# Kernel optimization log

Measured on AMD Instinct MI355X. Metric: run time of the kernel, lower is better.

Reference implementation:

```python
import jax, jax.numpy as jnp
import numpy as np
from jax import lax

N_QUANTIZE = 256
N_AUX = 28
N_RESCH = 512
N_SKIPCH = 256
KS = 2
DILATIONS = [2 ** i for i in range(10)] * 3  # 30 layers
L = len(DILATIONS)


def _causal_conv(x, w, b, d):
    # x: (B, Cin, T), w: (Cout, Cin, KS) torch Conv1d layout, left-pad => causal
    pad = (w.shape[-1] - 1) * d
    y = lax.conv_general_dilated(x, w, window_strides=(1,), padding=[(pad, 0)],
                                 rhs_dilation=(d,),
                                 dimension_numbers=('NCH', 'OIH', 'NCH'))
    return y + b[None, :, None]


def _conv1x1(x, w, b):
    # x: (B, Cin, T), w: (Cout, Cin)
    return jnp.einsum('oi,bit->bot', w, x) + b[None, :, None]


def setup_inputs() -> dict:
    key = jax.random.key(0)
    ks = jax.random.split(key, 20)
    B, T = 2, 8000
    s = 0.05
    rn = lambda k, shape: (jax.random.normal(k, shape, jnp.float32) * s)
    inp = {
        'x': jax.random.randint(ks[0], (B, T), 0, N_QUANTIZE),
        'h': jax.random.normal(ks[1], (B, N_AUX, T), jnp.float32),
        'causal_w': rn(ks[2], (N_RESCH, N_QUANTIZE, KS)),
        'causal_b': rn(ks[3], (N_RESCH,)),
        'dil_sig_w': rn(ks[4], (L, N_RESCH, N_RESCH, KS)),
        'dil_sig_b': rn(ks[5], (L, N_RESCH)),
        'dil_tanh_w': rn(ks[6], (L, N_RESCH, N_RESCH, KS)),
        'dil_tanh_b': rn(ks[7], (L, N_RESCH)),
        'aux_sig_w': rn(ks[8], (L, N_RESCH, N_AUX)),
        'aux_sig_b': rn(ks[9], (L, N_RESCH)),
        'aux_tanh_w': rn(ks[10], (L, N_RESCH, N_AUX)),
        'aux_tanh_b': rn(ks[11], (L, N_RESCH)),
        'skip_w': rn(ks[12], (L, N_SKIPCH, N_RESCH)),
        'skip_b': rn(ks[13], (L, N_SKIPCH)),
        'res_w': rn(ks[14], (L, N_RESCH, N_RESCH)),
        'res_b': rn(ks[15], (L, N_RESCH)),
        'post1_w': rn(ks[16], (N_SKIPCH, N_SKIPCH)),
        'post1_b': rn(ks[17], (N_SKIPCH,)),
        'post2_w': rn(ks[18], (N_QUANTIZE, N_SKIPCH)),
        'post2_b': rn(ks[19], (N_QUANTIZE,)),
    }
    return inp


def reference(x, h, causal_w, causal_b, dil_sig_w, dil_sig_b, dil_tanh_w, dil_tanh_b,
              aux_sig_w, aux_sig_b, aux_tanh_w, aux_tanh_b, skip_w, skip_b,
              res_w, res_b, post1_w, post1_b, post2_w, post2_b):
    B, T = x.shape
    # _preprocess: onehot (B,T,Q) -> (B,Q,T), then causal conv
    oh = jax.nn.one_hot(x % N_QUANTIZE, N_QUANTIZE, dtype=jnp.float32).transpose(0, 2, 1)
    out = _causal_conv(oh, causal_w, causal_b, 1)  # (B, n_resch, T)
    skip_sum = jnp.zeros((B, N_SKIPCH, T), jnp.float32)
    for l, d in enumerate(DILATIONS):
        sig = _causal_conv(out, dil_sig_w[l], dil_sig_b[l], d) + _conv1x1(h, aux_sig_w[l], aux_sig_b[l])
        tan = _causal_conv(out, dil_tanh_w[l], dil_tanh_b[l], d) + _conv1x1(h, aux_tanh_w[l], aux_tanh_b[l])
        z = jax.nn.sigmoid(sig) * jnp.tanh(tan)
        skip_sum = skip_sum + _conv1x1(z, skip_w[l], skip_b[l])
        out = _conv1x1(z, res_w[l], res_b[l]) + out
    # _postprocess: relu -> 1x1 -> relu -> 1x1 -> (B, T, n_quantize)
    y = jax.nn.relu(skip_sum)
    y = jax.nn.relu(_conv1x1(y, post1_w, post1_b))
    y = _conv1x1(y, post2_w, post2_b)
    return y.transpose(0, 2, 1)
```

## Files before the change

### kernel.cpp

```cpp
#include <hip/hip_runtime.h>
#include <math.h>

#define T_LEN 8000
#define BATCH 2
#define CCH 512
#define SKP 256
#define AUXP 32
#define NQ 256
#define NLAYER 30
#define PADF 512
#define TPAD 8192
#define ROWS (PADF + TPAD)
#define HROWS TPAD

typedef unsigned short hfu;
typedef unsigned int u32;
typedef __attribute__((ext_vector_type(8))) _Float16 half8;
typedef __attribute__((ext_vector_type(4))) float f32x4;

#define GLOAD16(g, l)                                                          \
  __builtin_amdgcn_global_load_lds(                                            \
      (const __attribute__((address_space(1))) void*)(g),                      \
      (__attribute__((address_space(3))) void*)(l), 16, 0, 0)

__device__ inline hfu hfbits(float f) {
  union { _Float16 h; hfu u; } x;
  x.h = (_Float16)f;
  return x.u;
}
__device__ inline u32 pk2(float a, float b) {
  return (u32)hfbits(a) | ((u32)hfbits(b) << 16);
}
__device__ inline uint4 pk8(const float f[8]) {
  return make_uint4(pk2(f[0], f[1]), pk2(f[2], f[3]), pk2(f[4], f[5]), pk2(f[6], f[7]));
}
__device__ inline int ldsL(int row, int ck) {
  return ((row >> 1) << 3) + ((((ck) ^ ((row >> 1) & 3)) << 1) | (row & 1));
}

__global__ __launch_bounds__(256) void zero16(uint4* p, int n) {
  for (int i = blockIdx.x * 256 + threadIdx.x; i < n; i += gridDim.x * 256)
    p[i] = make_uint4(0u, 0u, 0u, 0u);
}

__global__ __launch_bounds__(256) void cvt_dil(const float* __restrict__ in, hfu* __restrict__ out) {
  const long NG = (long)NLAYER * CCH * (CCH / 4);
  for (long g = (long)blockIdx.x * 256 + threadIdx.x; g < NG; g += (long)gridDim.x * 256) {
    const int i4 = (int)(g & 127) * 4;
    const int o = (int)((g >> 7) & 511);
    const int l = (int)(g >> 16);
    const float* pp = in + (((size_t)l * CCH + o) * CCH + i4) * 2;
    float4 f0 = *(const float4*)pp;
    float4 f1 = *(const float4*)(pp + 4);
    uint2 t0 = make_uint2(pk2(f0.x, f0.z), pk2(f1.x, f1.z));
    uint2 t1 = make_uint2(pk2(f0.y, f0.w), pk2(f1.y, f1.w));
    hfu* ob = out + ((size_t)l * 2 * CCH + o) * CCH + i4;
    *(uint2*)ob = t0;
    *(uint2*)(ob + (size_t)CCH * CCH) = t1;
  }
}

__global__ __launch_bounds__(256) void cvt_skipres(const float* __restrict__ skw,
                                                   const float* __restrict__ rsw,
                                                   hfu* __restrict__ out) {
  const long NG = (long)NLAYER * 768 * (CCH / 4);
  for (long g = (long)blockIdx.x * 256 + threadIdx.x; g < NG; g += (long)gridDim.x * 256) {
    const int i4 = (int)(g & 127) * 4;
    const int r = (int)((g >> 7) % 768);
    const int l = (int)(g / (128 * 768));
    const float* src = (r < SKP) ? (skw + ((size_t)l * SKP + r) * CCH + i4)
                                 : (rsw + ((size_t)l * CCH + (r - SKP)) * CCH + i4);
    float4 f = *(const float4*)src;
    *(uint2*)(out + ((size_t)l * 768 + r) * CCH + i4) = make_uint2(pk2(f.x, f.y), pk2(f.z, f.w));
  }
}

__global__ __launch_bounds__(256) void cvt_aux(const float* __restrict__ in, hfu* __restrict__ out) {
  const int N = NLAYER * CCH * AUXP;
  for (int i = blockIdx.x * 256 + threadIdx.x; i < N; i += gridDim.x * 256) {
    const int j = i & 31;
    const int o = (i >> 5) & 511;
    const int l = i >> 14;
    float v = (j < 28) ? in[((size_t)l * CCH + o) * 28 + j] : 0.f;
    out[i] = hfbits(v);
  }
}

__global__ __launch_bounds__(256) void cvt_copy(const float* __restrict__ in, hfu* __restrict__ out, int n) {
  for (int i = blockIdx.x * 256 + threadIdx.x; i < n; i += gridDim.x * 256)
    out[i] = hfbits(in[i]);
}

__global__ __launch_bounds__(256) void cvt_cwt(const float* __restrict__ cw, float* __restrict__ out) {
  const int N = 2 * NQ * CCH;
  for (int i = blockIdx.x * 256 + threadIdx.x; i < N; i += gridDim.x * 256) {
    const int tap = i >> 17;
    const int r = i & 131071;
    const int xq = r >> 9;
    const int o = r & 511;
    out[i] = cw[((size_t)o * NQ + xq) * 2 + tap];
  }
}

__global__ __launch_bounds__(256) void htrans_kernel(const float* __restrict__ h, hfu* __restrict__ hbf) {
  const int b = blockIdx.y;
  const int t = blockIdx.x * 64 + (threadIdx.x & 63);
  const int j0 = threadIdx.x >> 6;
#pragma unroll
  for (int j = j0; j < AUXP; j += 4) {
    float v = (j < 28 && t < T_LEN) ? h[((size_t)b * 28 + j) * T_LEN + t] : 0.f;
    hbf[((size_t)b * HROWS + t) * AUXP + j] = hfbits(v);
  }
}

template <int PRE>
__global__ __launch_bounds__(256) void embed_kernel(const int* __restrict__ x,
                                                    const float* __restrict__ cwt,
                                                    const float* __restrict__ cb,
                                                    float* __restrict__ outf,
                                                    hfu* __restrict__ outb) {
  const int b = blockIdx.y;
  const int t = blockIdx.x * 4 + (threadIdx.x >> 6);
  const int o = (threadIdx.x & 63) * 8;
  const int xc = x[(size_t)b * T_LEN + t] & 255;
  const int xp = (t > 0) ? (x[(size_t)b * T_LEN + t - 1] & 255) : 0;
  const float won = (t > 0) ? 1.f : 0.f;
  const float* c1 = cwt + 131072 + (size_t)xc * CCH + o;
  const float* c0 = cwt + (size_t)xp * CCH + o;
  float v[8];
#pragma unroll
  for (int j = 0; j < 8; ++j) v[j] = cb[o + j] + c1[j] + won * c0[j];
  if (PRE) {
    *(uint4*)&outb[((size_t)b * ROWS + PADF + t) * CCH + o] = pk8(v);
  } else {
    float* po = outf + ((size_t)b * ROWS + PADF + t) * CCH + o;
    *(float4*)po = make_float4(v[0], v[1], v[2], v[3]);
    *(float4*)(po + 4) = make_float4(v[4], v[5], v[6], v[7]);
  }
}

template <int PRE>
__global__ __launch_bounds__(512, 2) void gate_kernel(
    const hfu* __restrict__ actb, const float* __restrict__ actf,
    const hfu* __restrict__ hbf,
    const void* __restrict__ wsp, const void* __restrict__ wtp,
    const hfu* __restrict__ auxs, const hfu* __restrict__ auxt,
    const float* __restrict__ bs1, const float* __restrict__ bs2,
    const float* __restrict__ bt1, const float* __restrict__ bt2,
    hfu* __restrict__ z, int d) {
  __shared__ uint4 sm[4096];
  const int tid = threadIdx.x;
  const int lane = tid & 63, wid = tid >> 6;
  const int wm = wid >> 2, wn = wid & 3;
  const int lr = lane & 15, lq = lane >> 4;

  const int n = blockIdx.x;
  const int f = (n & 7) * 32 + (n >> 3);
  const int tt = f >> 3, inner = f & 7;
  const int o0 = (inner >> 1) * 128;
  const int b = inner & 1;
  const int t0 = tt * 256;

  f32x4 accS[4][4] = {};
  f32x4 accT[4][4] = {};

  auto stage = [&](int ih, int p) {
    const int base = p * 2048;
    const int pr = tid >> 3, w = tid & 7;
    const int row = (pr << 1) | (w & 1);
    const int ck = (w >> 1) ^ (pr & 3);
    if (ih < 32) {
      const int tau = (ih < 16) ? 1 : 0;
      const int koff = (ih & 15) * 32;
      if (PRE) {
        const size_t wo = ((size_t)tau * CCH + o0 + row) * CCH + koff + ck * 8;
        GLOAD16((const hfu*)wsp + wo, &sm[base + tid]);
        GLOAD16((const hfu*)wtp + wo, &sm[base + 512 + tid]);
#pragma unroll
        for (int c = 0; c < 2; ++c) {
          const int s = c * 512 + tid;
          const int pr2 = s >> 3, w2 = s & 7;
          const int row2 = (pr2 << 1) | (w2 & 1);
          const int ck2 = (w2 >> 1) ^ (pr2 & 3);
          const hfu* ar = actb + ((size_t)b * ROWS + PADF + t0 + row2 - (tau ? 0 : d)) * CCH + koff + ck2 * 8;
          GLOAD16(ar, &sm[base + 1024 + s]);
        }
      } else {
        const float* wsf = (const float*)wsp;
        const float* wtf = (const float*)wtp;
        const size_t fb = ((size_t)(o0 + row) * CCH + koff + ck * 8) * 2;
        float vs[8], vt[8];
#pragma unroll
        for (int j = 0; j < 4; ++j) {
          float4 fs = *(const float4*)&wsf[fb + j * 4];
          float4 ft = *(const float4*)&wtf[fb + j * 4];
          vs[2 * j] = tau ? fs.y : fs.x;
          vs[2 * j + 1] = tau ? fs.w : fs.z;
          vt[2 * j] = tau ? ft.y : ft.x;
          vt[2 * j + 1] = tau ? ft.w : ft.z;
        }
        sm[base + tid] = pk8(vs);
        sm[base + 512 + tid] = pk8(vt);
#pragma unroll
        for (int c = 0; c < 2; ++c) {
          const int s = c * 512 + tid;
          const int pr2 = s >> 3, w2 = s & 7;
          const int row2 = (pr2 << 1) | (w2 & 1);
          const int ck2 = (w2 >> 1) ^ (pr2 & 3);
          const float* ar = actf + ((size_t)b * ROWS + PADF + t0 + row2 - (tau ? 0 : d)) * CCH + koff + ck2 * 8;
          float4 f0 = *(const float4*)&ar[0];
          float4 f1 = *(const float4*)&ar[4];
          float vb[8] = {f0.x, f0.y, f0.z, f0.w, f1.x, f1.y, f1.z, f1.w};
          sm[base + 1024 + s] = pk8(vb);
        }
      }
    } else {
      if (PRE) {
        GLOAD16(auxs + (size_t)(o0 + row) * AUXP + ck * 8, &sm[base + tid]);
        GLOAD16(auxt + (size_t)(o0 + row) * AUXP + ck * 8, &sm[base + 512 + tid]);
      } else {
        sm[base + tid] = *(const uint4*)&auxs[(size_t)(o0 + row) * AUXP + ck * 8];
        sm[base + 512 + tid] = *(const uint4*)&auxt[(size_t)(o0 + row) * AUXP + ck * 8];
      }
#pragma unroll
      for (int c = 0; c < 2; ++c) {
        const int s = c * 512 + tid;
        const int pr2 = s >> 3, w2 = s & 7;
        const int row2 = (pr2 << 1) | (w2 & 1);
        const int ck2 = (w2 >> 1) ^ (pr2 & 3);
        if (PRE)
          GLOAD16(hbf + ((size_t)b * HROWS + t0 + row2) * AUXP + ck2 * 8, &sm[base + 1024 + s]);
        else
          sm[base + 1024 + s] = *(const uint4*)&hbf[((size_t)b * HROWS + t0 + row2) * AUXP + ck2 * 8];
      }
    }
  };

  auto compute = [&](int p) {
    const int base = p * 2048;
    half8 af[4], ag[4], bv[4];
#pragma unroll
    for (int mr = 0; mr < 4; ++mr) {
      const int row = wm * 64 + mr * 16 + lr;
      const int idx = ldsL(row, lq);
      af[mr] = *(const half8*)&sm[base + idx];
      ag[mr] = *(const half8*)&sm[base + 512 + idx];
    }
#pragma unroll
    for (int nr = 0; nr < 4; ++nr) {
      const int row = wn * 64 + nr * 16 + lr;
      bv[nr] = *(const half8*)&sm[base + 1024 + ldsL(row, lq)];
    }
#pragma unroll
    for (int mr = 0; mr < 4; ++mr)
#pragma unroll
      for (int nr = 0; nr < 4; ++nr) {
        accS[mr][nr] = __builtin_amdgcn_mfma_f32_16x16x32_f16(af[mr], bv[nr], accS[mr][nr], 0, 0, 0);
        accT[mr][nr] = __builtin_amdgcn_mfma_f32_16x16x32_f16(ag[mr], bv[nr], accT[mr][nr], 0, 0, 0);
      }
  };

  if (PRE) {
    stage(0, 0);
    for (int ih = 0; ih < 33; ++ih) {
      if (ih < 32) {
        stage(ih + 1, (ih + 1) & 1);
        asm volatile("s_waitcnt vmcnt(4)" ::: "memory");
      } else {
        asm volatile("s_waitcnt vmcnt(0)" ::: "memory");
      }
      __builtin_amdgcn_s_barrier();
      __builtin_amdgcn_sched_barrier(0);
      __builtin_amdgcn_s_setprio(1);
      compute(ih & 1);
      __builtin_amdgcn_s_setprio(0);
      __builtin_amdgcn_sched_barrier(0);
      __builtin_amdgcn_s_barrier();
    }
  } else {
    for (int ih = 0; ih < 33; ++ih) {
      stage(ih, ih & 1);
      __syncthreads();
      compute(ih & 1);
      __syncthreads();
    }
  }

#pragma unroll
  for (int mr = 0; mr < 4; ++mr) {
    const int ob = o0 + wm * 64 + mr * 16 + lq * 4;
    float4 x1 = *(const float4*)&bs1[ob];
    float4 x2 = *(const float4*)&bs2[ob];
    float4 y1 = *(const float4*)&bt1[ob];
    float4 y2 = *(const float4*)&bt2[ob];
    const float sb[4] = {x1.x + x2.x, x1.y + x2.y, x1.z + x2.z, x1.w + x2.w};
    const float tb[4] = {y1.x + y2.x, y1.y + y2.y, y1.z + y2.z, y1.w + y2.w};
#pragma unroll
    for (int nr = 0; nr < 4; ++nr) {
      const int t = t0 + wn * 64 + nr * 16 + lr;
      float zv[4];
#pragma unroll
      for (int j = 0; j < 4; ++j) {
        float sv = accS[mr][nr][j] + sb[j];
        float tv = accT[mr][nr][j] + tb[j];
        float sg = __builtin_amdgcn_rcpf(1.f + __expf(-sv));
        float e2 = __expf(2.f * tv);
        float th = 1.f - 2.f * __builtin_amdgcn_rcpf(e2 + 1.f);
        zv[j] = sg * th;
      }
      *(uint2*)&z[((size_t)b * HROWS + t) * CCH + ob] = make_uint2(pk2(zv[0], zv[1]), pk2(zv[2], zv[3]));
    }
  }
}

template <int PRE>
__global__ __launch_bounds__(512, 4) void update_kernel(
    const hfu* __restrict__ z, const void* __restrict__ wp,
    const float* __restrict__ skwf, const float* __restrict__ rswf,
    const float* __restrict__ skb, const float* __restrict__ rsb,
    float* __restrict__ skip, float* __restrict__ outf, hfu* __restrict__ outb) {
  __shared__ uint4 sm[2048];
  const int tid = threadIdx.x;
  const int lane = tid & 63, wid = tid >> 6;
  const int wm = wid >> 1, wn = wid & 1;
  const int lr = lane & 15, lq = lane >> 4;

  const int n = blockIdx.x;
  const int xcd = n & 7, j = n >> 3;
  const int ttl = j / 12, inner = j % 12;
  const int tt = xcd * 8 + ttl;
  if (tt > 62) return;
  const int rg = inner >> 1, b = inner & 1;
  const int r0 = rg * 128;
  const int t0 = tt * 128;

  f32x4 acc[2][4] = {};

  auto stage_u = [&](int ih, int p) {
    const int base = p * 1024;
    const int pr = tid >> 3, w = tid & 7;
    const int row = (pr << 1) | (w & 1);
    const int ck = (w >> 1) ^ (pr & 3);
    const int k0 = ih * 32;
    if (PRE) {
      GLOAD16((const hfu*)wp + (size_t)(r0 + row) * CCH + k0 + ck * 8, &sm[base + tid]);
      GLOAD16(z + ((size_t)b * HROWS + t0 + row) * CCH + k0 + ck * 8, &sm[base + 512 + tid]);
    } else {
      const int R = r0 + row;
      const float* src = (R < SKP) ? (skwf + (size_t)R * CCH + k0 + ck * 8)
                                   : (rswf + (size_t)(R - SKP) * CCH + k0 + ck * 8);
      float4 f0 = *(const float4*)&src[0];
      float4 f1 = *(const float4*)&src[4];
      float v[8] = {f0.x, f0.y, f0.z, f0.w, f1.x, f1.y, f1.z, f1.w};
      sm[base + tid] = pk8(v);
      sm[base + 512 + tid] = *(const uint4*)&z[((size_t)b * HROWS + t0 + row) * CCH + k0 + ck * 8];
    }
  };

  auto compute_u = [&](int p) {
    const int base = p * 1024;
    half8 av[2], bv[4];
#pragma unroll
    for (int mr = 0; mr < 2; ++mr) {
      const int row = wm * 32 + mr * 16 + lr;
      av[mr] = *(const half8*)&sm[base + ldsL(row, lq)];
    }
#pragma unroll
    for (int nr = 0; nr < 4; ++nr) {
      const int row = wn * 64 + nr * 16 + lr;
      bv[nr] = *(const half8*)&sm[base + 512 + ldsL(row, lq)];
    }
#pragma unroll
    for (int mr = 0; mr < 2; ++mr)
#pragma unroll
      for (int nr = 0; nr < 4; ++nr)
        acc[mr][nr] = __builtin_amdgcn_mfma_f32_16x16x32_f16(av[mr], bv[nr], acc[mr][nr], 0, 0, 0);
  };

  if (PRE) {
    stage_u(0, 0);
    for (int ih = 0; ih < 16; ++ih) {
      if (ih < 15) {
        stage_u(ih + 1, (ih + 1) & 1);
        asm volatile("s_waitcnt vmcnt(2)" ::: "memory");
      } else {
        asm volatile("s_waitcnt vmcnt(0)" ::: "memory");
      }
      __builtin_amdgcn_s_barrier();
      __builtin_amdgcn_sched_barrier(0);
      __builtin_amdgcn_s_setprio(1);
      compute_u(ih & 1);
      __builtin_amdgcn_s_setprio(0);
      __builtin_amdgcn_sched_barrier(0);
      __builtin_amdgcn_s_barrier();
    }
  } else {
    for (int ih = 0; ih < 16; ++ih) {
      stage_u(ih, ih & 1);
      __syncthreads();
      compute_u(ih & 1);
      __syncthreads();
    }
  }

  const bool iskip = (r0 < SKP);
#pragma unroll
  for (int mr = 0; mr < 2; ++mr) {
    const int R = r0 + wm * 32 + mr * 16 + lq * 4;
#pragma unroll
    for (int nr = 0; nr < 4; ++nr) {
      const int t = t0 + wn * 64 + nr * 16 + lr;
      if (t < T_LEN) {
        if (iskip) {
          float4 bb = *(const float4*)&skb[R];
          float4* p = (float4*)&skip[((size_t)b * T_LEN + t) * SKP + R];
          float4 v = *p;
          v.x += acc[mr][nr][0] + bb.x;
          v.y += acc[mr][nr][1] + bb.y;
          v.z += acc[mr][nr][2] + bb.z;
          v.w += acc[mr][nr][3] + bb.w;
          *p = v;
        } else {
          const int rr = R - SKP;
          float4 bb = *(const float4*)&rsb[rr];
          if (PRE) {
            hfu* pb = &outb[((size_t)b * ROWS + PADF + t) * CCH + rr];
            uint2 old = *(uint2*)pb;
            const _Float16* hp = (const _Float16*)&old;
            float v0 = (float)hp[0] + acc[mr][nr][0] + bb.x;
            float v1 = (float)hp[1] + acc[mr][nr][1] + bb.y;
            float v2 = (float)hp[2] + acc[mr][nr][2] + bb.z;
            float v3 = (float)hp[3] + acc[mr][nr][3] + bb.w;
            *(uint2*)pb = make_uint2(pk2(v0, v1), pk2(v2, v3));
          } else {
            float4* p = (float4*)&outf[((size_t)b * ROWS + PADF + t) * CCH + rr];
            float4 v = *p;
            v.x += acc[mr][nr][0] + bb.x;
            v.y += acc[mr][nr][1] + bb.y;
            v.z += acc[mr][nr][2] + bb.z;
            v.w += acc[mr][nr][3] + bb.w;
            *p = v;
          }
        }
      }
    }
  }
}

__global__ __launch_bounds__(256, 2) void post1_kernel(const float* __restrict__ skip,
                                                       const hfu* __restrict__ w,
                                                       const float* __restrict__ bias,
                                                       hfu* __restrict__ y1) {
  __shared__ uint4 sm[2048];
  uint4* sA = sm;
  uint4* sB = sm + 1024;
  const int tid = threadIdx.x;
  const int lane = tid & 63, wid = tid >> 6;
  const int wm = wid >> 1, wn = wid & 1;
  const int lr = lane & 15, lq = lane >> 4;
  const int t0 = blockIdx.x * 128;
  const int r0 = blockIdx.y * 128;
  const int b = blockIdx.z;
  f32x4 acc[4][4] = {};
  for (int kt = 0; kt < 4; ++kt) {
#pragma unroll
    for (int c = 0; c < 4; ++c) {
      const int cb = c * 256 + wid * 64;
      const int ch = cb + lane;
      const int ksub = ch >> 7, mn = ch & 127;
      const int k0 = kt * 64 + ksub * 8;
      GLOAD16(w + (size_t)(r0 + mn) * SKP + k0, &sA[cb]);
      int row = t0 + mn;
      if (row > T_LEN - 1) row = T_LEN - 1;
      const float* src = skip + ((size_t)b * T_LEN + row) * SKP + k0;
      float4 f0 = *(const float4*)&src[0];
      float4 f1 = *(const float4*)&src[4];
      float v[8] = {fmaxf(f0.x, 0.f), fmaxf(f0.y, 0.f), fmaxf(f0.z, 0.f), fmaxf(f0.w, 0.f),
                    fmaxf(f1.x, 0.f), fmaxf(f1.y, 0.f), fmaxf(f1.z, 0.f), fmaxf(f1.w, 0.f)};
      sB[ch] = pk8(v);
    }
    __syncthreads();
#pragma unroll
    for (int ks = 0; ks < 2; ++ks) {
      const int kb = (ks * 4 + lq) * 128;
      half8 av[4], bv[4];
#pragma unroll
      for (int r = 0; r < 4; ++r) {
        av[r] = *(const half8*)&sA[kb + wm * 64 + r * 16 + lr];
        bv[r] = *(const half8*)&sB[kb + wn * 64 + r * 16 + lr];
      }
#pragma unroll
      for (int mr = 0; mr < 4; ++mr)
#pragma unroll
        for (int nr = 0; nr < 4; ++nr)
          acc[mr][nr] = __builtin_amdgcn_mfma_f32_16x16x32_f16(av[mr], bv[nr], acc[mr][nr], 0, 0, 0);
    }
    __syncthreads();
  }
#pragma unroll
  for (int mr = 0; mr < 4; ++mr) {
    const int ob = r0 + wm * 64 + mr * 16 + lq * 4;
    float4 bb = *(const float4*)&bias[ob];
    const float bs[4] = {bb.x, bb.y, bb.z, bb.w};
#pragma unroll
    for (int nr = 0; nr < 4; ++nr) {
      const int t = t0 + wn * 64 + nr * 16 + lr;
      float v[4];
#pragma unroll
      for (int j = 0; j < 4; ++j) v[j] = fmaxf(acc[mr][nr][j] + bs[j], 0.f);
      *(uint2*)&y1[((size_t)b * HROWS + t) * SKP + ob] = make_uint2(pk2(v[0], v[1]), pk2(v[2], v[3]));
    }
  }
}

__global__ __launch_bounds__(256, 2) void post2_kernel(const hfu* __restrict__ y1,
                                                       const hfu* __restrict__ w,
                                                       const float* __restrict__ bias,
                                                       float* __restrict__ outp) {
  __shared__ uint4 sm[2048];
  uint4* sA = sm;
  uint4* sB = sm + 1024;
  const int tid = threadIdx.x;
  const int lane = tid & 63, wid = tid >> 6;
  const int wm = wid >> 1, wn = wid & 1;
  const int lr = lane & 15, lq = lane >> 4;
  const int t0 = blockIdx.x * 128;
  const int r0 = blockIdx.y * 128;
  const int b = blockIdx.z;
  f32x4 acc[4][4] = {};
  for (int kt = 0; kt < 4; ++kt) {
#pragma unroll
    for (int c = 0; c < 4; ++c) {
      const int cb = c * 256 + wid * 64;
      const int ch = cb + lane;
      const int ksub = ch >> 7, mn = ch & 127;
      const int k0 = kt * 64 + ksub * 8;
      GLOAD16(w + (size_t)(r0 + mn) * SKP + k0, &sA[cb]);
      GLOAD16(y1 + ((size_t)b * HROWS + t0 + mn) * SKP + k0, &sB[cb]);
    }
    __syncthreads();
#pragma unroll
    for (int ks = 0; ks < 2; ++ks) {
      const int kb = (ks * 4 + lq) * 128;
      half8 av[4], bv[4];
#pragma unroll
      for (int r = 0; r < 4; ++r) {
        av[r] = *(const half8*)&sA[kb + wm * 64 + r * 16 + lr];
        bv[r] = *(const half8*)&sB[kb + wn * 64 + r * 16 + lr];
      }
#pragma unroll
      for (int mr = 0; mr < 4; ++mr)
#pragma unroll
        for (int nr = 0; nr < 4; ++nr)
          acc[mr][nr] = __builtin_amdgcn_mfma_f32_16x16x32_f16(av[mr], bv[nr], acc[mr][nr], 0, 0, 0);
    }
    __syncthreads();
  }
#pragma unroll
  for (int mr = 0; mr < 4; ++mr) {
    const int ob = r0 + wm * 64 + mr * 16 + lq * 4;
    float4 bb = *(const float4*)&bias[ob];
#pragma unroll
    for (int nr = 0; nr < 4; ++nr) {
      const int t = t0 + wn * 64 + nr * 16 + lr;
      if (t < T_LEN) {
        float4 v;
        v.x = acc[mr][nr][0] + bb.x;
        v.y = acc[mr][nr][1] + bb.y;
        v.z = acc[mr][nr][2] + bb.z;
        v.w = acc[mr][nr][3] + bb.w;
        *(float4*)&outp[((size_t)b * T_LEN + t) * NQ + ob] = v;
      }
    }
  }
}

extern "C" void kernel_launch(void* const* d_in, const int* in_sizes, int n_in,
                              void* d_out, int out_size, void* d_ws, size_t ws_size,
                              hipStream_t stream) {
  const int* x = (const int*)d_in[0];
  const float* h = (const float*)d_in[1];
  const float* causal_w = (const float*)d_in[2];
  const float* causal_b = (const float*)d_in[3];
  const float* dil_sig_w = (const float*)d_in[4];
  const float* dil_sig_b = (const float*)d_in[5];
  const float* dil_tanh_w = (const float*)d_in[6];
  const float* dil_tanh_b = (const float*)d_in[7];
  const float* aux_sig_w = (const float*)d_in[8];
  const float* aux_sig_b = (const float*)d_in[9];
  const float* aux_tanh_w = (const float*)d_in[10];
  const float* aux_tanh_b = (const float*)d_in[11];
  const float* skip_w = (const float*)d_in[12];
  const float* skip_b = (const float*)d_in[13];
  const float* res_w = (const float*)d_in[14];
  const float* res_b = (const float*)d_in[15];
  const float* post1_w = (const float*)d_in[16];
  const float* post1_b = (const float*)d_in[17];
  const float* post2_w = (const float*)d_in[18];
  const float* post2_b = (const float*)d_in[19];
  float* outp = (float*)d_out;

  char* p = (char*)d_ws;
  auto alloc = [&](size_t bytes) {
    char* r = p;
    p += (bytes + 255) & ~(size_t)255;
    return r;
  };
  float* outf = (float*)alloc((size_t)BATCH * ROWS * CCH * 4);
  float* skip = (float*)alloc((size_t)BATCH * T_LEN * SKP * 4);
  hfu* zb = (hfu*)alloc((size_t)BATCH * HROWS * CCH * 2);
  hfu* hbf = (hfu*)alloc((size_t)BATCH * HROWS * AUXP * 2);
  hfu* auxsb = (hfu*)alloc((size_t)NLAYER * CCH * AUXP * 2);
  hfu* auxtb = (hfu*)alloc((size_t)NLAYER * CCH * AUXP * 2);
  hfu* p1b = (hfu*)alloc((size_t)NQ * SKP * 2);
  hfu* p2b = (hfu*)alloc((size_t)NQ * SKP * 2);
  float* cwt = (float*)alloc((size_t)2 * NQ * CCH * 4);
  hfu* y1 = zb;
  hfu* outb = (hfu*)alloc((size_t)BATCH * ROWS * CCH * 2);
  hfu* dilS = (hfu*)alloc((size_t)NLAYER * 2 * CCH * CCH * 2);
  hfu* dilT = (hfu*)alloc((size_t)NLAYER * 2 * CCH * CCH * 2);
  hfu* wsr = (hfu*)alloc((size_t)NLAYER * 768 * CCH * 2);
  const bool pre = ((size_t)(p - (char*)d_ws) <= ws_size);

  cvt_aux<<<256, 256, 0, stream>>>(aux_sig_w, auxsb);
  cvt_aux<<<256, 256, 0, stream>>>(aux_tanh_w, auxtb);
  cvt_copy<<<64, 256, 0, stream>>>(post1_w, p1b, NQ * SKP);
  cvt_copy<<<64, 256, 0, stream>>>(post2_w, p2b, NQ * SKP);
  cvt_cwt<<<1024, 256, 0, stream>>>(causal_w, cwt);
  if (pre) {
    cvt_dil<<<2048, 256, 0, stream>>>(dil_sig_w, dilS);
    cvt_dil<<<2048, 256, 0, stream>>>(dil_tanh_w, dilT);
    cvt_skipres<<<2048, 256, 0, stream>>>(skip_w, res_w, wsr);
  }

  zero16<<<512, 256, 0, stream>>>((uint4*)skip, (int)((size_t)BATCH * T_LEN * SKP * 4 / 16));
  for (int b = 0; b < BATCH; ++b) {
    if (pre) {
      zero16<<<32, 256, 0, stream>>>((uint4*)(outb + (size_t)b * ROWS * CCH), PADF * CCH * 2 / 16);
      zero16<<<48, 256, 0, stream>>>((uint4*)(outb + ((size_t)b * ROWS + PADF + T_LEN) * CCH),
                                     (TPAD - T_LEN) * CCH * 2 / 16);
    } else {
      zero16<<<64, 256, 0, stream>>>((uint4*)(outf + (size_t)b * ROWS * CCH), PADF * CCH * 4 / 16);
      zero16<<<96, 256, 0, stream>>>((uint4*)(outf + ((size_t)b * ROWS + PADF + T_LEN) * CCH),
                                     (TPAD - T_LEN) * CCH * 4 / 16);
    }
  }

  htrans_kernel<<<dim3(128, 2), 256, 0, stream>>>(h, hbf);
  if (pre)
    embed_kernel<1><<<dim3(2000, 2), 256, 0, stream>>>(x, cwt, causal_b, nullptr, outb);
  else
    embed_kernel<0><<<dim3(2000, 2), 256, 0, stream>>>(x, cwt, causal_b, outf, nullptr);

  for (int l = 0; l < NLAYER; ++l) {
    const int d = 1 << (l % 10);
    if (pre) {
      gate_kernel<1><<<256, 512, 0, stream>>>(
          outb, nullptr, hbf, dilS + (size_t)l * 2 * CCH * CCH, dilT + (size_t)l * 2 * CCH * CCH,
          auxsb + (size_t)l * CCH * AUXP, auxtb + (size_t)l * CCH * AUXP,
          dil_sig_b + (size_t)l * CCH, aux_sig_b + (size_t)l * CCH,
          dil_tanh_b + (size_t)l * CCH, aux_tanh_b + (size_t)l * CCH, zb, d);
      update_kernel<1><<<768, 512, 0, stream>>>(
          zb, wsr + (size_t)l * 768 * CCH, nullptr, nullptr,
          skip_b + (size_t)l * SKP, res_b + (size_t)l * CCH, skip, nullptr, outb);
    } else {
      gate_kernel<0><<<256, 512, 0, stream>>>(
          nullptr, outf, hbf, dil_sig_w + (size_t)l * CCH * CCH * 2,
          dil_tanh_w + (size_t)l * CCH * CCH * 2,
          auxsb + (size_t)l * CCH * AUXP, auxtb + (size_t)l * CCH * AUXP,
          dil_sig_b + (size_t)l * CCH, aux_sig_b + (size_t)l * CCH,
          dil_tanh_b + (size_t)l * CCH, aux_tanh_b + (size_t)l * CCH, zb, d);
      update_kernel<0><<<768, 512, 0, stream>>>(
          zb, nullptr, skip_w + (size_t)l * SKP * CCH, res_w + (size_t)l * CCH * CCH,
          skip_b + (size_t)l * SKP, res_b + (size_t)l * CCH, skip, outf, nullptr);
    }
  }

  post1_kernel<<<dim3(63, 2, BATCH), 256, 0, stream>>>(skip, p1b, post1_b, y1);
  post2_kernel<<<dim3(63, 2, BATCH), 256, 0, stream>>>(y1, p2b, post2_b, outp);
}
```

Measured before the change: 2.166 ms.

## Double gate K-tile to 64 with dynamic LDS, store skip sum in fp16, fuse dil conversion

The gate kernel now stages 64-wide K chunks (16 dilated iterations plus one aux step instead of 33) into 128 KB of dynamic shared memory with a new XOR swizzle. This halves the number of barriers and pipeline steps per tile. The skip accumulator becomes fp16 in the pre-converted path, halving its read-modify-write traffic in every layer's update kernel, at some cost in accumulation precision. The two dilated-weight conversion launches are merged into one. The larger LDS footprint may lower occupancy from the declared 2 blocks per CU.

```diff
diff --git a/kernel.cpp b/kernel.cpp
--- a/kernel.cpp
+++ b/kernel.cpp
@@ -43,9 +43,15 @@
     p[i] = make_uint4(0u, 0u, 0u, 0u);
 }
 
-__global__ __launch_bounds__(256) void cvt_dil(const float* __restrict__ in, hfu* __restrict__ out) {
+__global__ __launch_bounds__(256) void cvt_dil2(const float* __restrict__ inS,
+                                                const float* __restrict__ inT,
+                                                hfu* __restrict__ outS, hfu* __restrict__ outT) {
   const long NG = (long)NLAYER * CCH * (CCH / 4);
-  for (long g = (long)blockIdx.x * 256 + threadIdx.x; g < NG; g += (long)gridDim.x * 256) {
+  for (long g2 = (long)blockIdx.x * 256 + threadIdx.x; g2 < 2 * NG; g2 += (long)gridDim.x * 256) {
+    const int sel = (int)(g2 >= NG);
+    const long g = sel ? (g2 - NG) : g2;
+    const float* in = sel ? inT : inS;
+    hfu* out = sel ? outT : outS;
     const int i4 = (int)(g & 127) * 4;
     const int o = (int)((g >> 7) & 511);
     const int l = (int)(g >> 16);
@@ -148,7 +154,7 @@
     const float* __restrict__ bs1, const float* __restrict__ bs2,
     const float* __restrict__ bt1, const float* __restrict__ bt2,
     hfu* __restrict__ z, int d) {
-  __shared__ uint4 sm[4096];
+  extern __shared__ uint4 smd[];
   const int tid = threadIdx.x;
   const int lane = tid & 63, wid = tid >> 6;
   const int wm = wid >> 2, wn = wid & 3;
@@ -164,30 +170,33 @@
   f32x4 accS[4][4] = {};
   f32x4 accT[4][4] = {};
 
-  auto stage = [&](int ih, int p) {
-    const int base = p * 2048;
-    const int pr = tid >> 3, w = tid & 7;
-    const int row = (pr << 1) | (w & 1);
-    const int ck = (w >> 1) ^ (pr & 3);
-    if (ih < 32) {
-      const int tau = (ih < 16) ? 1 : 0;
-      const int koff = (ih & 15) * 32;
-      if (PRE) {
+  auto stage_dil = [&](int ih, int p) {
+    const int base = p * 4096;
+    const int tau = (ih < 8) ? 1 : 0;
+    const int koff = (ih & 7) * 64;
+    if (PRE) {
+#pragma unroll
+      for (int c = 0; c < 2; ++c) {
+        const int s = c * 512 + tid;
+        const int row = s >> 3, ck = (s & 7) ^ (row & 7);
         const size_t wo = ((size_t)tau * CCH + o0 + row) * CCH + koff + ck * 8;
-        GLOAD16((const hfu*)wsp + wo, &sm[base + tid]);
-        GLOAD16((const hfu*)wtp + wo, &sm[base + 512 + tid]);
-#pragma unroll
-        for (int c = 0; c < 2; ++c) {
-          const int s = c * 512 + tid;
-          const int pr2 = s >> 3, w2 = s & 7;
-          const int row2 = (pr2 << 1) | (w2 & 1);
-          const int ck2 = (w2 >> 1) ^ (pr2 & 3);
-          const hfu* ar = actb + ((size_t)b * ROWS + PADF + t0 + row2 - (tau ? 0 : d)) * CCH + koff + ck2 * 8;
-          GLOAD16(ar, &sm[base + 1024 + s]);
-        }
-      } else {
-        const float* wsf = (const float*)wsp;
-        const float* wtf = (const float*)wtp;
+        GLOAD16((const hfu*)wsp + wo, &smd[base + s]);
+        GLOAD16((const hfu*)wtp + wo, &smd[base + 1024 + s]);
+      }
+#pragma unroll
+      for (int c = 0; c < 4; ++c) {
+        const int s = c * 512 + tid;
+        const int row = s >> 3, ck = (s & 7) ^ (row & 7);
+        const hfu* ar = actb + ((size_t)b * ROWS + PADF + t0 + row - (tau ? 0 : d)) * CCH + koff + ck * 8;
+        GLOAD16(ar, &smd[base + 2048 + s]);
+      }
+    } else {
+      const float* wsf = (const float*)wsp;
+      const float* wtf = (const float*)wtp;
+#pragma unroll
+      for (int c = 0; c < 2; ++c) {
+        const int s = c * 512 + tid;
+        const int row = s >> 3, ck = (s & 7) ^ (row & 7);
         const size_t fb = ((size_t)(o0 + row) * CCH + koff + ck * 8) * 2;
         float vs[8], vt[8];
 #pragma unroll
@@ -199,57 +208,86 @@
           vt[2 * j] = tau ? ft.y : ft.x;
           vt[2 * j + 1] = tau ? ft.w : ft.z;
         }
-        sm[base + tid] = pk8(vs);
-        sm[base + 512 + tid] = pk8(vt);
-#pragma unroll
-        for (int c = 0; c < 2; ++c) {
-          const int s = c * 512 + tid;
-          const int pr2 = s >> 3, w2 = s & 7;
-          const int row2 = (pr2 << 1) | (w2 & 1);
-          const int ck2 = (w2 >> 1) ^ (pr2 & 3);
-          const float* ar = actf + ((size_t)b * ROWS + PADF + t0 + row2 - (tau ? 0 : d)) * CCH + koff + ck2 * 8;
-          float4 f0 = *(const float4*)&ar[0];
-          float4 f1 = *(const float4*)&ar[4];
-          float vb[8] = {f0.x, f0.y, f0.z, f0.w, f1.x, f1.y, f1.z, f1.w};
-          sm[base + 1024 + s] = pk8(vb);
+        smd[base + s] = pk8(vs);
+        smd[base + 1024 + s] = pk8(vt);
+      }
+#pragma unroll
+      for (int c = 0; c < 4; ++c) {
+        const int s = c * 512 + tid;
+        const int row = s >> 3, ck = (s & 7) ^ (row & 7);
+        const float* ar = actf + ((size_t)b * ROWS + PADF + t0 + row - (tau ? 0 : d)) * CCH + koff + ck * 8;
+        float4 f0 = *(const float4*)&ar[0];
+        float4 f1 = *(const float4*)&ar[4];
+        float vb[8] = {f0.x, f0.y, f0.z, f0.w, f1.x, f1.y, f1.z, f1.w};
+        smd[base + 2048 + s] = pk8(vb);
+      }
+    }
+  };
+
+  auto stage_aux = [&](int p) {
+    const int base = p * 4096;
+    {
+      const int row = tid >> 2, ck = (tid & 3) ^ (row & 3);
+      if (PRE) {
+        GLOAD16(auxs + (size_t)(o0 + row) * AUXP + ck * 8, &smd[base + tid]);
+        GLOAD16(auxt + (size_t)(o0 + row) * AUXP + ck * 8, &smd[base + 1024 + tid]);
+      } else {
+        smd[base + tid] = *(const uint4*)&auxs[(size_t)(o0 + row) * AUXP + ck * 8];
+        smd[base + 1024 + tid] = *(const uint4*)&auxt[(size_t)(o0 + row) * AUXP + ck * 8];
+      }
+    }
+#pragma unroll
+    for (int c = 0; c < 2; ++c) {
+      const int s = c * 512 + tid;
+      const int row = s >> 2, ck = (s & 3) ^ (row & 3);
+      if (PRE)
+        GLOAD16(hbf + ((size_t)b * HROWS + t0 + row) * AUXP + ck * 8, &smd[base + 2048 + s]);
+      else
+        smd[base + 2048 + s] = *(const uint4*)&hbf[((size_t)b * HROWS + t0 + row) * AUXP + ck * 8];
+    }
+  };
+
+  auto compute_dil = [&](int p) {
+    const int base = p * 4096;
+#pragma unroll
+    for (int kk = 0; kk < 2; ++kk) {
+      half8 af[4], ag[4], bv[4];
+#pragma unroll
+      for (int mr = 0; mr < 4; ++mr) {
+        const int row = wm * 64 + mr * 16 + lr;
+        const int idx = row * 8 + ((kk * 4 + lq) ^ (row & 7));
+        af[mr] = *(const half8*)&smd[base + idx];
+        ag[mr] = *(const half8*)&smd[base + 1024 + idx];
+      }
+#pragma unroll
+      for (int nr = 0; nr < 4; ++nr) {
+        const int row = wn * 64 + nr * 16 + lr;
+        bv[nr] = *(const half8*)&smd[base + 2048 + row * 8 + ((kk * 4 + lq) ^ (row & 7))];
+      }
+#pragma unroll
+      for (int mr = 0; mr < 4; ++mr)
+#pragma unroll
+        for (int nr = 0; nr < 4; ++nr) {
+          accS[mr][nr] = __builtin_amdgcn_mfma_f32_16x16x32_f16(af[mr], bv[nr], accS[mr][nr], 0, 0, 0);
+          accT[mr][nr] = __builtin_amdgcn_mfma_f32_16x16x32_f16(ag[mr], bv[nr], accT[mr][nr], 0, 0, 0);
         }
-      }
-    } else {
-      if (PRE) {
-        GLOAD16(auxs + (size_t)(o0 + row) * AUXP + ck * 8, &sm[base + tid]);
-        GLOAD16(auxt + (size_t)(o0 + row) * AUXP + ck * 8, &sm[base + 512 + tid]);
-      } else {
-        sm[base + tid] = *(const uint4*)&auxs[(size_t)(o0 + row) * AUXP + ck * 8];
-        sm[base + 512 + tid] = *(const uint4*)&auxt[(size_t)(o0 + row) * AUXP + ck * 8];
-      }
-#pragma unroll
-      for (int c = 0; c < 2; ++c) {
-        const int s = c * 512 + tid;
-        const int pr2 = s >> 3, w2 = s & 7;
-        const int row2 = (pr2 << 1) | (w2 & 1);
-        const int ck2 = (w2 >> 1) ^ (pr2 & 3);
-        if (PRE)
-          GLOAD16(hbf + ((size_t)b * HROWS + t0 + row2) * AUXP + ck2 * 8, &sm[base + 1024 + s]);
-        else
-          sm[base + 1024 + s] = *(const uint4*)&hbf[((size_t)b * HROWS + t0 + row2) * AUXP + ck2 * 8];
-      }
     }
   };
 
-  auto compute = [&](int p) {
-    const int base = p * 2048;
+  auto compute_aux = [&](int p) {
+    const int base = p * 4096;
     half8 af[4], ag[4], bv[4];
 #pragma unroll
     for (int mr = 0; mr < 4; ++mr) {
       const int row = wm * 64 + mr * 16 + lr;
-      const int idx = ldsL(row, lq);
-      af[mr] = *(const half8*)&sm[base + idx];
-      ag[mr] = *(const half8*)&sm[base + 512 + idx];
+      const int idx = row * 4 + (lq ^ (row & 3));
+      af[mr] = *(const half8*)&smd[base + idx];
+      ag[mr] = *(const half8*)&smd[base + 1024 + idx];
     }
 #pragma unroll
     for (int nr = 0; nr < 4; ++nr) {
       const int row = wn * 64 + nr * 16 + lr;
-      bv[nr] = *(const half8*)&sm[base + 1024 + ldsL(row, lq)];
+      bv[nr] = *(const half8*)&smd[base + 2048 + row * 4 + (lq ^ (row & 3))];
     }
 #pragma unroll
     for (int mr = 0; mr < 4; ++mr)
@@ -261,10 +299,13 @@
   };
 
   if (PRE) {
-    stage(0, 0);
-    for (int ih = 0; ih < 33; ++ih) {
-      if (ih < 32) {
-        stage(ih + 1, (ih + 1) & 1);
+    stage_dil(0, 0);
+    for (int ih = 0; ih < 17; ++ih) {
+      if (ih < 15) {
+        stage_dil(ih + 1, (ih + 1) & 1);
+        asm volatile("s_waitcnt vmcnt(8)" ::: "memory");
+      } else if (ih == 15) {
+        stage_aux(0);
         asm volatile("s_waitcnt vmcnt(4)" ::: "memory");
       } else {
         asm volatile("s_waitcnt vmcnt(0)" ::: "memory");
@@ -272,16 +313,16 @@
       __builtin_amdgcn_s_barrier();
       __builtin_amdgcn_sched_barrier(0);
       __builtin_amdgcn_s_setprio(1);
-      compute(ih & 1);
+      if (ih < 16) compute_dil(ih & 1); else compute_aux(0);
       __builtin_amdgcn_s_setprio(0);
       __builtin_amdgcn_sched_barrier(0);
       __builtin_amdgcn_s_barrier();
     }
   } else {
-    for (int ih = 0; ih < 33; ++ih) {
-      stage(ih, ih & 1);
+    for (int ih = 0; ih < 17; ++ih) {
+      if (ih < 16) stage_dil(ih, ih & 1); else stage_aux(0);
       __syncthreads();
-      compute(ih & 1);
+      if (ih < 16) compute_dil(ih & 1); else compute_aux(0);
       __syncthreads();
     }
   }
@@ -318,7 +359,8 @@
     const hfu* __restrict__ z, const void* __restrict__ wp,
     const float* __restrict__ skwf, const float* __restrict__ rswf,
     const float* __restrict__ skb, const float* __restrict__ rsb,
-    float* __restrict__ skip, float* __restrict__ outf, hfu* __restrict__ outb) {
+    float* __restrict__ skip, hfu* __restrict__ skiph,
+    float* __restrict__ outf, hfu* __restrict__ outb) {
   __shared__ uint4 sm[2048];
   const int tid = threadIdx.x;
   const int lane = tid & 63, wid = tid >> 6;
@@ -413,13 +455,24 @@
       if (t < T_LEN) {
         if (iskip) {
           float4 bb = *(const float4*)&skb[R];
-          float4* p = (float4*)&skip[((size_t)b * T_LEN + t) * SKP + R];
-          float4 v = *p;
-          v.x += acc[mr][nr][0] + bb.x;
-          v.y += acc[mr][nr][1] + bb.y;
-          v.z += acc[mr][nr][2] + bb.z;
-          v.w += acc[mr][nr][3] + bb.w;
-          *p = v;
+          if (PRE) {
+            hfu* ps = &skiph[((size_t)b * T_LEN + t) * SKP + R];
+            uint2 old = *(uint2*)ps;
+            const _Float16* hp = (const _Float16*)&old;
+            float v0 = (float)hp[0] + acc[mr][nr][0] + bb.x;
+            float v1 = (float)hp[1] + acc[mr][nr][1] + bb.y;
+            float v2 = (float)hp[2] + acc[mr][nr][2] + bb.z;
+            float v3 = (float)hp[3] + acc[mr][nr][3] + bb.w;
+            *(uint2*)ps = make_uint2(pk2(v0, v1), pk2(v2, v3));
+          } else {
+            float4* p = (float4*)&skip[((size_t)b * T_LEN + t) * SKP + R];
+            float4 v = *p;
+            v.x += acc[mr][nr][0] + bb.x;
+            v.y += acc[mr][nr][1] + bb.y;
+            v.z += acc[mr][nr][2] + bb.z;
+            v.w += acc[mr][nr][3] + bb.w;
+            *p = v;
+          }
         } else {
           const int rr = R - SKP;
           float4 bb = *(const float4*)&rsb[rr];
@@ -447,7 +500,9 @@
   }
 }
 
+template <int PRE>
 __global__ __launch_bounds__(256, 2) void post1_kernel(const float* __restrict__ skip,
+                                                       const hfu* __restrict__ skiph,
                                                        const hfu* __restrict__ w,
                                                        const float* __restrict__ bias,
                                                        hfu* __restrict__ y1) {
@@ -472,12 +527,21 @@
       GLOAD16(w + (size_t)(r0 + mn) * SKP + k0, &sA[cb]);
       int row = t0 + mn;
       if (row > T_LEN - 1) row = T_LEN - 1;
-      const float* src = skip + ((size_t)b * T_LEN + row) * SKP + k0;
-      float4 f0 = *(const float4*)&src[0];
-      float4 f1 = *(const float4*)&src[4];
-      float v[8] = {fmaxf(f0.x, 0.f), fmaxf(f0.y, 0.f), fmaxf(f0.z, 0.f), fmaxf(f0.w, 0.f),
-                    fmaxf(f1.x, 0.f), fmaxf(f1.y, 0.f), fmaxf(f1.z, 0.f), fmaxf(f1.w, 0.f)};
-      sB[ch] = pk8(v);
+      if (PRE) {
+        uint4 u = *(const uint4*)&skiph[((size_t)b * T_LEN + row) * SKP + k0];
+        const _Float16* hp = (const _Float16*)&u;
+        float v[8];
+#pragma unroll
+        for (int j = 0; j < 8; ++j) v[j] = fmaxf((float)hp[j], 0.f);
+        sB[ch] = pk8(v);
+      } else {
+        const float* src = skip + ((size_t)b * T_LEN + row) * SKP + k0;
+        float4 f0 = *(const float4*)&src[0];
+        float4 f1 = *(const float4*)&src[4];
+        float v[8] = {fmaxf(f0.x, 0.f), fmaxf(f0.y, 0.f), fmaxf(f0.z, 0.f), fmaxf(f0.w, 0.f),
+                      fmaxf(f1.x, 0.f), fmaxf(f1.y, 0.f), fmaxf(f1.z, 0.f), fmaxf(f1.w, 0.f)};
+        sB[ch] = pk8(v);
+      }
     }
     __syncthreads();
 #pragma unroll
@@ -600,6 +664,11 @@
   const float* post2_b = (const float*)d_in[19];
   float* outp = (float*)d_out;
 
+  hipFuncSetAttribute((const void*)gate_kernel<1>,
+                      hipFuncAttributeMaxDynamicSharedMemorySize, 131072);
+  hipFuncSetAttribute((const void*)gate_kernel<0>,
+                      hipFuncAttributeMaxDynamicSharedMemorySize, 131072);
+
   char* p = (char*)d_ws;
   auto alloc = [&](size_t bytes) {
     char* r = p;
@@ -615,6 +684,7 @@
   hfu* p1b = (hfu*)alloc((size_t)NQ * SKP * 2);
   hfu* p2b = (hfu*)alloc((size_t)NQ * SKP * 2);
   float* cwt = (float*)alloc((size_t)2 * NQ * CCH * 4);
+  hfu* skiph = (hfu*)alloc((size_t)BATCH * T_LEN * SKP * 2);
   hfu* y1 = zb;
   hfu* outb = (hfu*)alloc((size_t)BATCH * ROWS * CCH * 2);
   hfu* dilS = (hfu*)alloc((size_t)NLAYER * 2 * CCH * CCH * 2);
@@ -628,18 +698,20 @@
   cvt_copy<<<64, 256, 0, stream>>>(post2_w, p2b, NQ * SKP);
   cvt_cwt<<<1024, 256, 0, stream>>>(causal_w, cwt);
   if (pre) {
-    cvt_dil<<<2048, 256, 0, stream>>>(dil_sig_w, dilS);
-    cvt_dil<<<2048, 256, 0, stream>>>(dil_tanh_w, dilT);
+    cvt_dil2<<<4096, 256, 0, stream>>>(dil_sig_w, dil_tanh_w, dilS, dilT);
     cvt_skipres<<<2048, 256, 0, stream>>>(skip_w, res_w, wsr);
   }
 
-  zero16<<<512, 256, 0, stream>>>((uint4*)skip, (int)((size_t)BATCH * T_LEN * SKP * 4 / 16));
-  for (int b = 0; b < BATCH; ++b) {
-    if (pre) {
+  if (pre) {
+    zero16<<<512, 256, 0, stream>>>((uint4*)skiph, (int)((size_t)BATCH * T_LEN * SKP * 2 / 16));
+    for (int b = 0; b < BATCH; ++b) {
       zero16<<<32, 256, 0, stream>>>((uint4*)(outb + (size_t)b * ROWS * CCH), PADF * CCH * 2 / 16);
       zero16<<<48, 256, 0, stream>>>((uint4*)(outb + ((size_t)b * ROWS + PADF + T_LEN) * CCH),
                                      (TPAD - T_LEN) * CCH * 2 / 16);
-    } else {
+    }
+  } else {
+    zero16<<<512, 256, 0, stream>>>((uint4*)skip, (int)((size_t)BATCH * T_LEN * SKP * 4 / 16));
+    for (int b = 0; b < BATCH; ++b) {
       zero16<<<64, 256, 0, stream>>>((uint4*)(outf + (size_t)b * ROWS * CCH), PADF * CCH * 4 / 16);
       zero16<<<96, 256, 0, stream>>>((uint4*)(outf + ((size_t)b * ROWS + PADF + T_LEN) * CCH),
                                      (TPAD - T_LEN) * CCH * 4 / 16);
@@ -655,16 +727,16 @@
   for (int l = 0; l < NLAYER; ++l) {
     const int d = 1 << (l % 10);
     if (pre) {
-      gate_kernel<1><<<256, 512, 0, stream>>>(
+      gate_kernel<1><<<256, 512, 131072, stream>>>(
           outb, nullptr, hbf, dilS + (size_t)l * 2 * CCH * CCH, dilT + (size_t)l * 2 * CCH * CCH,
           auxsb + (size_t)l * CCH * AUXP, auxtb + (size_t)l * CCH * AUXP,
           dil_sig_b + (size_t)l * CCH, aux_sig_b + (size_t)l * CCH,
           dil_tanh_b + (size_t)l * CCH, aux_tanh_b + (size_t)l * CCH, zb, d);
       update_kernel<1><<<768, 512, 0, stream>>>(
           zb, wsr + (size_t)l * 768 * CCH, nullptr, nullptr,
-          skip_b + (size_t)l * SKP, res_b + (size_t)l * CCH, skip, nullptr, outb);
+          skip_b + (size_t)l * SKP, res_b + (size_t)l * CCH, nullptr, skiph, nullptr, outb);
     } else {
-      gate_kernel<0><<<256, 512, 0, stream>>>(
+      gate_kernel<0><<<256, 512, 131072, stream>>>(
           nullptr, outf, hbf, dil_sig_w + (size_t)l * CCH * CCH * 2,
           dil_tanh_w + (size_t)l * CCH * CCH * 2,
           auxsb + (size_t)l * CCH * AUXP, auxtb + (size_t)l * CCH * AUXP,
@@ -672,10 +744,13 @@
           dil_tanh_b + (size_t)l * CCH, aux_tanh_b + (size_t)l * CCH, zb, d);
       update_kernel<0><<<768, 512, 0, stream>>>(
           zb, nullptr, skip_w + (size_t)l * SKP * CCH, res_w + (size_t)l * CCH * CCH,
-          skip_b + (size_t)l * SKP, res_b + (size_t)l * CCH, skip, outf, nullptr);
-    }
-  }
-
-  post1_kernel<<<dim3(63, 2, BATCH), 256, 0, stream>>>(skip, p1b, post1_b, y1);
+          skip_b + (size_t)l * SKP, res_b + (size_t)l * CCH, skip, nullptr, outf, nullptr);
+    }
+  }
+
+  if (pre)
+    post1_kernel<1><<<dim3(63, 2, BATCH), 256, 0, stream>>>(nullptr, skiph, p1b, post1_b, y1);
+  else
+    post1_kernel<0><<<dim3(63, 2, BATCH), 256, 0, stream>>>(skip, nullptr, p1b, post1_b, y1);
   post2_kernel<<<dim3(63, 2, BATCH), 256, 0, stream>>>(y1, p2b, post2_b, outp);
 }
```

New measurement: 2.087 ms. 1.04x faster.
